# Kernel optimization log

Hardware: AMD Instinct MI355X
Metric: run time of the kernel (lower is better)

Reference implementation:

```python
import jax, jax.numpy as jnp
import numpy as np

N_PTS = 500000
R = 8            # channels per plane (num_channels=24 // 3)
FEAT = 24        # concat of 3 planes
HID = 168        # mlp_dim
OUT = 35
SIZES = [128, 256, 512]  # plane resolutions per level (plane_size=512, level_factor=0.5)
XYZ_MIN, XYZ_MAX = -2.0, 2.0


def setup_inputs() -> dict:
    key = jax.random.key(0)
    ks = jax.random.split(key, 64)
    inp = {"xyz": jax.random.uniform(ks[0], (N_PTS, 3), dtype=jnp.float32)}
    ki = 1
    for i, s in enumerate(SIZES):
        # planes stored [R, H, W]; torch init randn*0.1
        inp[f"xy{i}"] = jax.random.normal(ks[ki + 0], (R, s, s), dtype=jnp.float32) * 0.1
        inp[f"xz{i}"] = jax.random.normal(ks[ki + 1], (R, s, s), dtype=jnp.float32) * 0.1
        inp[f"yz{i}"] = jax.random.normal(ks[ki + 2], (R, s, s), dtype=jnp.float32) * 0.1
        inp[f"w1_{i}"] = jax.random.normal(ks[ki + 3], (FEAT, HID), dtype=jnp.float32) * 0.05
        inp[f"b1_{i}"] = jnp.zeros((HID,), jnp.float32)
        inp[f"w2_{i}"] = jax.random.normal(ks[ki + 4], (HID, HID), dtype=jnp.float32) * 0.05
        inp[f"b2_{i}"] = jnp.zeros((HID,), jnp.float32)
        inp[f"w3_{i}"] = jax.random.normal(ks[ki + 5], (HID, OUT), dtype=jnp.float32) * 0.05
        inp[f"b3_{i}"] = jnp.zeros((OUT,), jnp.float32)
        ki += 6
    return inp


def _bilinear(plane, gx, gy):
    # plane: [C,H,W]; gx in [-1,1] maps to W, gy maps to H; align_corners=True
    C, H, W = plane.shape
    ix = (gx + 1.0) * 0.5 * (W - 1)
    iy = (gy + 1.0) * 0.5 * (H - 1)
    x0 = jnp.floor(ix).astype(jnp.int32)
    y0 = jnp.floor(iy).astype(jnp.int32)
    wx = ix - x0
    wy = iy - y0
    x0c = jnp.clip(x0, 0, W - 1); x1c = jnp.clip(x0 + 1, 0, W - 1)
    y0c = jnp.clip(y0, 0, H - 1); y1c = jnp.clip(y0 + 1, 0, H - 1)
    v00 = plane[:, y0c, x0c]  # [C,N]
    v01 = plane[:, y0c, x1c]
    v10 = plane[:, y1c, x0c]
    v11 = plane[:, y1c, x1c]
    top = v00 * (1 - wx) + v01 * wx
    bot = v10 * (1 - wx) + v11 * wx
    return (top * (1 - wy) + bot * wy).T  # [N,C]


def _forward(xyz, planes, mlps):
    nrm = (xyz - XYZ_MIN) / (XYZ_MAX - XYZ_MIN) * 2.0 - 1.0  # [N,3]
    nx, ny, nz = nrm[:, 0], nrm[:, 1], nrm[:, 2]
    tmp = 0.0
    for (xy, xz, yz), (w1, b1, w2, b2, w3, b3) in zip(planes, mlps):
        # xy_plane[H=X,W=Y] sampled with grid (gx=ny, gy=nx), etc.
        feat = jnp.concatenate([
            _bilinear(xy, ny, nx),
            _bilinear(xz, nz, nx),
            _bilinear(yz, nz, ny),
        ], axis=-1)  # [N,24]
        h = jax.nn.relu(feat @ w1 + b1)
        h = jax.nn.relu(h @ w2 + b2)
        tmp = tmp + (h @ w3 + b3)
    # inference head: features[:27], rotations[27:31] raw; scale sigmoid; opacity*10
    return jnp.concatenate([tmp[:, :31], jax.nn.sigmoid(tmp[:, 31:34]), tmp[:, 34:] * 10.0], axis=-1)


def reference(xyz, xy0, xz0, yz0, w1_0, b1_0, w2_0, b2_0, w3_0, b3_0,
              xy1, xz1, yz1, w1_1, b1_1, w2_1, b2_1, w3_1, b3_1,
              xy2, xz2, yz2, w1_2, b1_2, w2_2, b2_2, w3_2, b3_2):
    planes = [(xy0, xz0, yz0), (xy1, xz1, yz1), (xy2, xz2, yz2)]
    mlps = [(w1_0, b1_0, w2_0, b2_0, w3_0, b3_0),
            (w1_1, b1_1, w2_1, b2_1, w3_1, b3_1),
            (w1_2, b1_2, w2_2, b2_2, w3_2, b3_2)]
    return _forward(xyz, planes, mlps)
```

## Files before the change

kernel.cpp:

```cpp
#include <hip/hip_runtime.h>

#define N_PTS 500000
#define FEAT 24
#define HID 168
#define OUT_C 35
#define MT 64
#define H_STR 176
#define WREG (32 * H_STR + 16)

#define WF1_OFF 0
#define WF2_OFF 18432
#define WF3_OFF 129024
#define W_TOTAL 156672
#define PL_S0 (W_TOTAL)
#define PL_S1 (PL_S0 + 393216)
#define PL_S2 (PL_S1 + 1572864)

typedef short bf16x8 __attribute__((ext_vector_type(8)));
typedef float f32x4 __attribute__((ext_vector_type(4)));

__device__ __forceinline__ unsigned short f2bf(float f) {
    union { float f; unsigned int u; } v; v.f = f;
    unsigned int u = v.u;
    return (unsigned short)((u + 0x7FFFu + ((u >> 16) & 1u)) >> 16);
}
__device__ __forceinline__ float bf2f(unsigned short h) {
    union { unsigned int u; float f; } v; v.u = ((unsigned int)h) << 16;
    return v.f;
}
__device__ __forceinline__ unsigned int pk_bf16(float a, float b) {
    unsigned int r;
    asm("v_cvt_pk_bf16_f32 %0, %1, %2" : "=v"(r) : "v"(a), "v"(b));
    return r;
}
__device__ __forceinline__ f32x4 mfma16(bf16x8 a, bf16x8 b, f32x4 c) {
    return __builtin_amdgcn_mfma_f32_16x16x32_bf16(a, b, c, 0, 0, 0);
}

__global__ __launch_bounds__(256) void prep_weights(
    const float* __restrict__ w1a, const float* __restrict__ w2a, const float* __restrict__ w3a,
    const float* __restrict__ w1b, const float* __restrict__ w2b, const float* __restrict__ w3b,
    const float* __restrict__ w1c, const float* __restrict__ w2c, const float* __restrict__ w3c,
    unsigned short* __restrict__ ws)
{
    int id = blockIdx.x * 256 + threadIdx.x;
    if (id >= W_TOTAL) return;
    const float* w1[3] = {w1a, w1b, w1c};
    const float* w2[3] = {w2a, w2b, w2c};
    const float* w3[3] = {w3a, w3b, w3c};
    float v = 0.f;
    if (id < WF2_OFF) {
        int s = id / 6144, r = id % 6144;
        int mt = r >> 9, q = r & 511, lane = q >> 3, j = q & 7;
        int n = mt * 16 + (lane & 15), k = (lane >> 4) * 8 + j;
        if (n < HID && k < FEAT) v = w1[s][k * HID + n];
    } else if (id < WF3_OFF) {
        int t = id - WF2_OFF;
        int s = t / 36864, r = t % 36864;
        int fi = r >> 9, q = r & 511, lane = q >> 3, j = q & 7;
        int kk = fi / 12, mt = fi % 12;
        int n = mt * 16 + (lane & 15), k = kk * 32 + (lane >> 4) * 8 + j;
        if (n < HID && k < HID) v = w2[s][k * HID + n];
    } else {
        int t = id - WF3_OFF;
        int s = t / 9216, r = t % 9216;
        int fi = r >> 9, q = r & 511, lane = q >> 3, j = q & 7;
        int mt = fi / 6, kk = fi % 6;
        int n = mt * 16 + (lane & 15), k = kk * 32 + (lane >> 4) * 8 + j;
        if (n < OUT_C && k < HID) v = w3[s][k * OUT_C + n];
    }
    ws[id] = f2bf(v);
}

__global__ __launch_bounds__(256) void prep_planes(
    const float* __restrict__ xy0, const float* __restrict__ xz0, const float* __restrict__ yz0,
    const float* __restrict__ xy1, const float* __restrict__ xz1, const float* __restrict__ yz1,
    const float* __restrict__ xy2, const float* __restrict__ xz2, const float* __restrict__ yz2,
    unsigned short* __restrict__ ws)
{
    const float* pls[9] = {xy0, xz0, yz0, xy1, xz1, yz1, xy2, xz2, yz2};
    int b = blockIdx.x;
    int s, pl, chunk, SS, base;
    if (b < 192)        { s = 0; SS = 16384;  pl = b / 64;   chunk = b % 64;    base = PL_S0; }
    else if (b < 960)   { int t = b - 192; s = 1; SS = 65536;  pl = t / 256;  chunk = t % 256;  base = PL_S1; }
    else                { int t = b - 960; s = 2; SS = 262144; pl = t / 1024; chunk = t % 1024; base = PL_S2; }
    const float* src = pls[s * 3 + pl];
    int pos = chunk * 256 + threadIdx.x;
    uint4 pk;
    unsigned int* po = (unsigned int*)&pk;
    #pragma unroll
    for (int c = 0; c < 4; ++c) {
        float f0 = src[(2 * c)     * SS + pos];
        float f1 = src[(2 * c + 1) * SS + pos];
        po[c] = pk_bf16(f0, f1);
    }
    *reinterpret_cast<uint4*>(&ws[base + pl * SS * 8 + pos * 8]) = pk;
}

__global__ __launch_bounds__(128, 4) void tri_mlp(
    const float* __restrict__ xyz,
    const float* __restrict__ b1_0, const float* __restrict__ b2_0, const float* __restrict__ b3_0,
    const float* __restrict__ b1_1, const float* __restrict__ b2_1, const float* __restrict__ b3_1,
    const float* __restrict__ b1_2, const float* __restrict__ b2_2, const float* __restrict__ b3_2,
    const unsigned short* __restrict__ wpack,
    float* __restrict__ out)
{
    __shared__ __align__(16) unsigned short H[2 * WREG];

    const int tid  = threadIdx.x;
    const int wave = tid >> 6;
    const int lane = tid & 63;
    const int quad = lane >> 4;
    const int l16  = lane & 15;
    const int p0   = blockIdx.x * MT;
    const int prow = wave * 32;
    unsigned short* Hw = H + wave * WREG;

    if (lane < 8) ((unsigned int*)(Hw + 32 * H_STR))[lane] = 0u;

    float X[2], Y[2], Z[2];
    #pragma unroll
    for (int ni = 0; ni < 2; ++ni) {
        int gp = min(p0 + prow + ni * 16 + l16, N_PTS - 1);
        X[ni] = xyz[gp * 3 + 0];
        Y[ni] = xyz[gp * 3 + 1];
        Z[ni] = xyz[gp * 3 + 2];
    }

    f32x4 c3[2][3];
    #pragma unroll
    for (int mt = 0; mt < 3; ++mt) {
        f32x4 cb;
        #pragma unroll
        for (int r = 0; r < 4; ++r) {
            int ch = mt * 16 + quad * 4 + r;
            cb[r] = (ch < OUT_C) ? (b3_0[ch] + b3_1[ch] + b3_2[ch]) : 0.f;
        }
        c3[0][mt] = cb;
        c3[1][mt] = cb;
    }

    #pragma unroll 1
    for (int s = 0; s < 3; ++s) {
        const float *b1, *b2;
        int S, sbase;
        if (s == 0)      { b1 = b1_0; b2 = b2_0; S = 128; sbase = PL_S0; }
        else if (s == 1) { b1 = b1_1; b2 = b2_1; S = 256; sbase = PL_S1; }
        else             { b1 = b1_2; b2 = b2_2; S = 512; sbase = PL_S2; }

        bf16x8 B1[2];
        #pragma unroll
        for (int ni = 0; ni < 2; ++ni) {
            uint4 pk = {0u, 0u, 0u, 0u};
            if (quad < 3) {
                float gx, gy;
                if (quad == 0)      { gx = Y[ni]; gy = X[ni]; }
                else if (quad == 1) { gx = Z[ni]; gy = X[ni]; }
                else                { gx = Z[ni]; gy = Y[ni]; }
                gx *= 0.5f; gy *= 0.5f;
                float ix = (gx + 1.0f) * 0.5f * (float)(S - 1);
                float iy = (gy + 1.0f) * 0.5f * (float)(S - 1);
                float fx = floorf(ix), fy = floorf(iy);
                int x0 = (int)fx, y0 = (int)fy;
                float wx = ix - fx, wy = iy - fy;
                int x0c = min(max(x0, 0), S - 1);
                int x1c = min(x0 + 1, S - 1);
                int y0c = min(max(y0, 0), S - 1);
                int y1c = min(y0 + 1, S - 1);
                const unsigned short* pcl = wpack + sbase + (quad << 3) * S * S;
                uint4 q00 = *(const uint4*)&pcl[(y0c * S + x0c) * 8];
                uint4 q01 = *(const uint4*)&pcl[(y0c * S + x1c) * 8];
                uint4 q10 = *(const uint4*)&pcl[(y1c * S + x0c) * 8];
                uint4 q11 = *(const uint4*)&pcl[(y1c * S + x1c) * 8];
                float w00 = (1.f - wx) * (1.f - wy), w01 = wx * (1.f - wy);
                float w10 = (1.f - wx) * wy,         w11 = wx * wy;
                const unsigned int* u00 = (const unsigned int*)&q00;
                const unsigned int* u01 = (const unsigned int*)&q01;
                const unsigned int* u10 = (const unsigned int*)&q10;
                const unsigned int* u11 = (const unsigned int*)&q11;
                unsigned int* po = (unsigned int*)&pk;
                #pragma unroll
                for (int h = 0; h < 4; ++h) {
                    float a0 = bf2f((unsigned short)(u00[h] & 0xFFFF)) * w00
                             + bf2f((unsigned short)(u01[h] & 0xFFFF)) * w01
                             + bf2f((unsigned short)(u10[h] & 0xFFFF)) * w10
                             + bf2f((unsigned short)(u11[h] & 0xFFFF)) * w11;
                    float a1 = bf2f((unsigned short)(u00[h] >> 16)) * w00
                             + bf2f((unsigned short)(u01[h] >> 16)) * w01
                             + bf2f((unsigned short)(u10[h] >> 16)) * w10
                             + bf2f((unsigned short)(u11[h] >> 16)) * w11;
                    po[h] = pk_bf16(a0, a1);
                }
            }
            B1[ni] = *reinterpret_cast<bf16x8*>(&pk);
        }

        {
            const unsigned short* w1f = wpack + WF1_OFF + s * 6144;
            #pragma unroll
            for (int mt = 0; mt < 11; ++mt) {
                bf16x8 a = *(const bf16x8*)&w1f[mt * 512 + lane * 8];
                float4 bias = *(const float4*)&b1[min(mt * 16 + quad * 4, HID - 4)];
                f32x4 cb = {bias.x, bias.y, bias.z, bias.w};
                #pragma unroll
                for (int ni = 0; ni < 2; ++ni) {
                    f32x4 c = mfma16(a, B1[ni], cb);
                    unsigned int u0 = pk_bf16(fmaxf(c[0], 0.f), fmaxf(c[1], 0.f));
                    unsigned int u1 = pk_bf16(fmaxf(c[2], 0.f), fmaxf(c[3], 0.f));
                    *reinterpret_cast<uint2*>(&Hw[(ni * 16 + l16) * H_STR + mt * 16 + quad * 4]) =
                        make_uint2(u0, u1);
                }
            }
        }

        bf16x8 B2[2][6];
        #pragma unroll
        for (int ni = 0; ni < 2; ++ni)
            #pragma unroll
            for (int kk = 0; kk < 6; ++kk)
                B2[ni][kk] = *(const bf16x8*)&Hw[(ni * 16 + l16) * H_STR + kk * 32 + quad * 8];

        {
            const unsigned short* w2f = wpack + WF2_OFF + s * 36864;
            #pragma unroll 1
            for (int mt = 0; mt < 11; ++mt) {
                float4 bias = *(const float4*)&b2[min(mt * 16 + quad * 4, HID - 4)];
                f32x4 c20 = {bias.x, bias.y, bias.z, bias.w};
                f32x4 c21 = c20;
                #pragma unroll
                for (int kk = 0; kk < 6; ++kk) {
                    bf16x8 a = *(const bf16x8*)&w2f[(kk * 12 + mt) * 512 + lane * 8];
                    c20 = mfma16(a, B2[0][kk], c20);
                    c21 = mfma16(a, B2[1][kk], c21);
                }
                unsigned int u00 = pk_bf16(fmaxf(c20[0], 0.f), fmaxf(c20[1], 0.f));
                unsigned int u01 = pk_bf16(fmaxf(c20[2], 0.f), fmaxf(c20[3], 0.f));
                *reinterpret_cast<uint2*>(&Hw[(l16) * H_STR + mt * 16 + quad * 4]) =
                    make_uint2(u00, u01);
                unsigned int u10 = pk_bf16(fmaxf(c21[0], 0.f), fmaxf(c21[1], 0.f));
                unsigned int u11 = pk_bf16(fmaxf(c21[2], 0.f), fmaxf(c21[3], 0.f));
                *reinterpret_cast<uint2*>(&Hw[(16 + l16) * H_STR + mt * 16 + quad * 4]) =
                    make_uint2(u10, u11);
            }
        }

        {
            const unsigned short* w3f = wpack + WF3_OFF + s * 9216;
            #pragma unroll 1
            for (int kk = 0; kk < 6; ++kk) {
                bf16x8 b30 = *(const bf16x8*)&Hw[(l16) * H_STR + kk * 32 + quad * 8];
                bf16x8 b31 = *(const bf16x8*)&Hw[(16 + l16) * H_STR + kk * 32 + quad * 8];
                #pragma unroll
                for (int mt = 0; mt < 3; ++mt) {
                    bf16x8 a = *(const bf16x8*)&w3f[(mt * 6 + kk) * 512 + lane * 8];
                    c3[0][mt] = mfma16(a, b30, c3[0][mt]);
                    c3[1][mt] = mfma16(a, b31, c3[1][mt]);
                }
            }
        }
    }

    float* Hf = (float*)Hw;
    #pragma unroll
    for (int ni = 0; ni < 2; ++ni) {
        int row = ni * 16 + l16;
        #pragma unroll
        for (int mt = 0; mt < 3; ++mt) {
            #pragma unroll
            for (int r = 0; r < 4; ++r) {
                int ch = mt * 16 + quad * 4 + r;
                if (ch < OUT_C) {
                    float v = c3[ni][mt][r];
                    if (ch >= 31 && ch < 34)      v = 1.0f / (1.0f + expf(-v));
                    else if (ch == 34)            v *= 10.0f;
                    Hf[row * 35 + ch] = v;
                }
            }
        }
    }
    if (p0 + prow < N_PTS) {
        const int base = (p0 + prow) * 35;
        #pragma unroll
        for (int t = 0; t < 5; ++t) {
            int off = t * 256 + lane * 4;
            if (off < 1120) {
                f32x4 v = *(const f32x4*)&Hf[off];
                __builtin_nontemporal_store(v, reinterpret_cast<f32x4*>(&out[base + off]));
            }
        }
    }
}

extern "C" void kernel_launch(void* const* d_in, const int* in_sizes, int n_in,
                              void* d_out, int out_size, void* d_ws, size_t ws_size,
                              hipStream_t stream) {
    (void)in_sizes; (void)n_in; (void)out_size; (void)ws_size;
    const float* xyz  = (const float*)d_in[0];
    const float* xy0  = (const float*)d_in[1];
    const float* xz0  = (const float*)d_in[2];
    const float* yz0  = (const float*)d_in[3];
    const float* w1_0 = (const float*)d_in[4];
    const float* b1_0 = (const float*)d_in[5];
    const float* w2_0 = (const float*)d_in[6];
    const float* b2_0 = (const float*)d_in[7];
    const float* w3_0 = (const float*)d_in[8];
    const float* b3_0 = (const float*)d_in[9];
    const float* xy1  = (const float*)d_in[10];
    const float* xz1  = (const float*)d_in[11];
    const float* yz1  = (const float*)d_in[12];
    const float* w1_1 = (const float*)d_in[13];
    const float* b1_1 = (const float*)d_in[14];
    const float* w2_1 = (const float*)d_in[15];
    const float* b2_1 = (const float*)d_in[16];
    const float* w3_1 = (const float*)d_in[17];
    const float* b3_1 = (const float*)d_in[18];
    const float* xy2  = (const float*)d_in[19];
    const float* xz2  = (const float*)d_in[20];
    const float* yz2  = (const float*)d_in[21];
    const float* w1_2 = (const float*)d_in[22];
    const float* b1_2 = (const float*)d_in[23];
    const float* w2_2 = (const float*)d_in[24];
    const float* b2_2 = (const float*)d_in[25];
    const float* w3_2 = (const float*)d_in[26];
    const float* b3_2 = (const float*)d_in[27];

    unsigned short* ws = (unsigned short*)d_ws;
    float* out = (float*)d_out;

    prep_weights<<<(W_TOTAL + 255) / 256, 256, 0, stream>>>(
        w1_0, w2_0, w3_0, w1_1, w2_1, w3_1, w1_2, w2_2, w3_2, ws);

    prep_planes<<<4032, 256, 0, stream>>>(
        xy0, xz0, yz0, xy1, xz1, yz1, xy2, xz2, yz2, ws);

    tri_mlp<<<(N_PTS + MT - 1) / MT, 128, 0, stream>>>(
        xyz,
        b1_0, b2_0, b3_0, b1_1, b2_1, b3_1, b1_2, b2_2, b3_2,
        ws, out);
}
```

Before: 374.2 us.

## Fold MLP biases into padded weight K-slot and merge prep kernels

```diff
diff --git a/kernel.cpp b/kernel.cpp
--- a/kernel.cpp
+++ b/kernel.cpp
@@ -16,6 +16,8 @@
 #define PL_S1 (PL_S0 + 393216)
 #define PL_S2 (PL_S1 + 1572864)
 
+#define PREP_W_BLOCKS 612
+
 typedef short bf16x8 __attribute__((ext_vector_type(8)));
 typedef float f32x4 __attribute__((ext_vector_type(4)));
 
@@ -37,49 +39,62 @@
     return __builtin_amdgcn_mfma_f32_16x16x32_bf16(a, b, c, 0, 0, 0);
 }
 
-__global__ __launch_bounds__(256) void prep_weights(
+__global__ __launch_bounds__(256) void prep_all(
+    const float* __restrict__ xy0, const float* __restrict__ xz0, const float* __restrict__ yz0,
+    const float* __restrict__ xy1, const float* __restrict__ xz1, const float* __restrict__ yz1,
+    const float* __restrict__ xy2, const float* __restrict__ xz2, const float* __restrict__ yz2,
     const float* __restrict__ w1a, const float* __restrict__ w2a, const float* __restrict__ w3a,
     const float* __restrict__ w1b, const float* __restrict__ w2b, const float* __restrict__ w3b,
     const float* __restrict__ w1c, const float* __restrict__ w2c, const float* __restrict__ w3c,
+    const float* __restrict__ b1a, const float* __restrict__ b2a, const float* __restrict__ b3a,
+    const float* __restrict__ b1b, const float* __restrict__ b2b, const float* __restrict__ b3b,
+    const float* __restrict__ b1c, const float* __restrict__ b2c, const float* __restrict__ b3c,
     unsigned short* __restrict__ ws)
 {
-    int id = blockIdx.x * 256 + threadIdx.x;
-    if (id >= W_TOTAL) return;
-    const float* w1[3] = {w1a, w1b, w1c};
-    const float* w2[3] = {w2a, w2b, w2c};
-    const float* w3[3] = {w3a, w3b, w3c};
-    float v = 0.f;
-    if (id < WF2_OFF) {
-        int s = id / 6144, r = id % 6144;
-        int mt = r >> 9, q = r & 511, lane = q >> 3, j = q & 7;
-        int n = mt * 16 + (lane & 15), k = (lane >> 4) * 8 + j;
-        if (n < HID && k < FEAT) v = w1[s][k * HID + n];
-    } else if (id < WF3_OFF) {
-        int t = id - WF2_OFF;
-        int s = t / 36864, r = t % 36864;
-        int fi = r >> 9, q = r & 511, lane = q >> 3, j = q & 7;
-        int kk = fi / 12, mt = fi % 12;
-        int n = mt * 16 + (lane & 15), k = kk * 32 + (lane >> 4) * 8 + j;
-        if (n < HID && k < HID) v = w2[s][k * HID + n];
-    } else {
-        int t = id - WF3_OFF;
-        int s = t / 9216, r = t % 9216;
-        int fi = r >> 9, q = r & 511, lane = q >> 3, j = q & 7;
-        int mt = fi / 6, kk = fi % 6;
-        int n = mt * 16 + (lane & 15), k = kk * 32 + (lane >> 4) * 8 + j;
-        if (n < OUT_C && k < HID) v = w3[s][k * OUT_C + n];
-    }
-    ws[id] = f2bf(v);
-}
-
-__global__ __launch_bounds__(256) void prep_planes(
-    const float* __restrict__ xy0, const float* __restrict__ xz0, const float* __restrict__ yz0,
-    const float* __restrict__ xy1, const float* __restrict__ xz1, const float* __restrict__ yz1,
-    const float* __restrict__ xy2, const float* __restrict__ xz2, const float* __restrict__ yz2,
-    unsigned short* __restrict__ ws)
-{
+    if (blockIdx.x < PREP_W_BLOCKS) {
+        int id = blockIdx.x * 256 + threadIdx.x;
+        const float* w1[3] = {w1a, w1b, w1c};
+        const float* w2[3] = {w2a, w2b, w2c};
+        const float* w3[3] = {w3a, w3b, w3c};
+        const float* b1[3] = {b1a, b1b, b1c};
+        const float* b2[3] = {b2a, b2b, b2c};
+        const float* b3[3] = {b3a, b3b, b3c};
+        float v = 0.f;
+        if (id < WF2_OFF) {
+            int s = id / 6144, r = id % 6144;
+            int mt = r >> 9, q = r & 511, lane = q >> 3, j = q & 7;
+            int n = mt * 16 + (lane & 15), k = (lane >> 4) * 8 + j;
+            if (n < HID) {
+                if (k < FEAT)       v = w1[s][k * HID + n];
+                else if (k == FEAT) v = b1[s][n];
+            }
+        } else if (id < WF3_OFF) {
+            int t = id - WF2_OFF;
+            int s = t / 36864, r = t % 36864;
+            int fi = r >> 9, q = r & 511, lane = q >> 3, j = q & 7;
+            int kk = fi / 12, mt = fi % 12;
+            int n = mt * 16 + (lane & 15), k = kk * 32 + (lane >> 4) * 8 + j;
+            if (n < HID) {
+                if (k < HID)        v = w2[s][k * HID + n];
+                else if (k == HID)  v = b2[s][n];
+            }
+        } else {
+            int t = id - WF3_OFF;
+            int s = t / 9216, r = t % 9216;
+            int fi = r >> 9, q = r & 511, lane = q >> 3, j = q & 7;
+            int mt = fi / 6, kk = fi % 6;
+            int n = mt * 16 + (lane & 15), k = kk * 32 + (lane >> 4) * 8 + j;
+            if (n < OUT_C) {
+                if (k < HID)        v = w3[s][k * OUT_C + n];
+                else if (k == HID)  v = b3[s][n];
+            }
+        }
+        ws[id] = f2bf(v);
+        return;
+    }
+
     const float* pls[9] = {xy0, xz0, yz0, xy1, xz1, yz1, xy2, xz2, yz2};
-    int b = blockIdx.x;
+    int b = blockIdx.x - PREP_W_BLOCKS;
     int s, pl, chunk, SS, base;
     if (b < 192)        { s = 0; SS = 16384;  pl = b / 64;   chunk = b % 64;    base = PL_S0; }
     else if (b < 960)   { int t = b - 192; s = 1; SS = 65536;  pl = t / 256;  chunk = t % 256;  base = PL_S1; }
@@ -99,9 +114,6 @@
 
 __global__ __launch_bounds__(128, 4) void tri_mlp(
     const float* __restrict__ xyz,
-    const float* __restrict__ b1_0, const float* __restrict__ b2_0, const float* __restrict__ b3_0,
-    const float* __restrict__ b1_1, const float* __restrict__ b2_1, const float* __restrict__ b3_1,
-    const float* __restrict__ b1_2, const float* __restrict__ b2_2, const float* __restrict__ b3_2,
     const unsigned short* __restrict__ wpack,
     float* __restrict__ out)
 {
@@ -116,6 +128,8 @@
     const int prow = wave * 32;
     unsigned short* Hw = H + wave * WREG;
 
+    if (lane < 32)
+        *reinterpret_cast<uint4*>(&Hw[lane * H_STR + HID]) = make_uint4(0x3F80u, 0u, 0u, 0u);
     if (lane < 8) ((unsigned int*)(Hw + 32 * H_STR))[lane] = 0u;
 
     float X[2], Y[2], Z[2];
@@ -130,28 +144,21 @@
     f32x4 c3[2][3];
     #pragma unroll
     for (int mt = 0; mt < 3; ++mt) {
-        f32x4 cb;
-        #pragma unroll
-        for (int r = 0; r < 4; ++r) {
-            int ch = mt * 16 + quad * 4 + r;
-            cb[r] = (ch < OUT_C) ? (b3_0[ch] + b3_1[ch] + b3_2[ch]) : 0.f;
-        }
-        c3[0][mt] = cb;
-        c3[1][mt] = cb;
+        c3[0][mt] = (f32x4){0.f, 0.f, 0.f, 0.f};
+        c3[1][mt] = (f32x4){0.f, 0.f, 0.f, 0.f};
     }
 
     #pragma unroll 1
     for (int s = 0; s < 3; ++s) {
-        const float *b1, *b2;
         int S, sbase;
-        if (s == 0)      { b1 = b1_0; b2 = b2_0; S = 128; sbase = PL_S0; }
-        else if (s == 1) { b1 = b1_1; b2 = b2_1; S = 256; sbase = PL_S1; }
-        else             { b1 = b1_2; b2 = b2_2; S = 512; sbase = PL_S2; }
+        if (s == 0)      { S = 128; sbase = PL_S0; }
+        else if (s == 1) { S = 256; sbase = PL_S1; }
+        else             { S = 512; sbase = PL_S2; }
 
         bf16x8 B1[2];
         #pragma unroll
         for (int ni = 0; ni < 2; ++ni) {
-            uint4 pk = {0u, 0u, 0u, 0u};
+            uint4 pk = {0x3F80u, 0u, 0u, 0u};
             if (quad < 3) {
                 float gx, gy;
                 if (quad == 0)      { gx = Y[ni]; gy = X[ni]; }
@@ -200,15 +207,14 @@
             #pragma unroll
             for (int mt = 0; mt < 11; ++mt) {
                 bf16x8 a = *(const bf16x8*)&w1f[mt * 512 + lane * 8];
-                float4 bias = *(const float4*)&b1[min(mt * 16 + quad * 4, HID - 4)];
-                f32x4 cb = {bias.x, bias.y, bias.z, bias.w};
                 #pragma unroll
                 for (int ni = 0; ni < 2; ++ni) {
-                    f32x4 c = mfma16(a, B1[ni], cb);
+                    f32x4 c = mfma16(a, B1[ni], (f32x4){0.f, 0.f, 0.f, 0.f});
                     unsigned int u0 = pk_bf16(fmaxf(c[0], 0.f), fmaxf(c[1], 0.f));
                     unsigned int u1 = pk_bf16(fmaxf(c[2], 0.f), fmaxf(c[3], 0.f));
-                    *reinterpret_cast<uint2*>(&Hw[(ni * 16 + l16) * H_STR + mt * 16 + quad * 4]) =
-                        make_uint2(u0, u1);
+                    if (mt < 10 || quad < 2)
+                        *reinterpret_cast<uint2*>(&Hw[(ni * 16 + l16) * H_STR + mt * 16 + quad * 4]) =
+                            make_uint2(u0, u1);
                 }
             }
         }
@@ -224,8 +230,7 @@
             const unsigned short* w2f = wpack + WF2_OFF + s * 36864;
             #pragma unroll 1
             for (int mt = 0; mt < 11; ++mt) {
-                float4 bias = *(const float4*)&b2[min(mt * 16 + quad * 4, HID - 4)];
-                f32x4 c20 = {bias.x, bias.y, bias.z, bias.w};
+                f32x4 c20 = {0.f, 0.f, 0.f, 0.f};
                 f32x4 c21 = c20;
                 #pragma unroll
                 for (int kk = 0; kk < 6; ++kk) {
@@ -233,14 +238,16 @@
                     c20 = mfma16(a, B2[0][kk], c20);
                     c21 = mfma16(a, B2[1][kk], c21);
                 }
-                unsigned int u00 = pk_bf16(fmaxf(c20[0], 0.f), fmaxf(c20[1], 0.f));
-                unsigned int u01 = pk_bf16(fmaxf(c20[2], 0.f), fmaxf(c20[3], 0.f));
-                *reinterpret_cast<uint2*>(&Hw[(l16) * H_STR + mt * 16 + quad * 4]) =
-                    make_uint2(u00, u01);
-                unsigned int u10 = pk_bf16(fmaxf(c21[0], 0.f), fmaxf(c21[1], 0.f));
-                unsigned int u11 = pk_bf16(fmaxf(c21[2], 0.f), fmaxf(c21[3], 0.f));
-                *reinterpret_cast<uint2*>(&Hw[(16 + l16) * H_STR + mt * 16 + quad * 4]) =
-                    make_uint2(u10, u11);
+                if (mt < 10 || quad < 2) {
+                    unsigned int u00 = pk_bf16(fmaxf(c20[0], 0.f), fmaxf(c20[1], 0.f));
+                    unsigned int u01 = pk_bf16(fmaxf(c20[2], 0.f), fmaxf(c20[3], 0.f));
+                    *reinterpret_cast<uint2*>(&Hw[(l16) * H_STR + mt * 16 + quad * 4]) =
+                        make_uint2(u00, u01);
+                    unsigned int u10 = pk_bf16(fmaxf(c21[0], 0.f), fmaxf(c21[1], 0.f));
+                    unsigned int u11 = pk_bf16(fmaxf(c21[2], 0.f), fmaxf(c21[3], 0.f));
+                    *reinterpret_cast<uint2*>(&Hw[(16 + l16) * H_STR + mt * 16 + quad * 4]) =
+                        make_uint2(u10, u11);
+                }
             }
         }
 
@@ -327,14 +334,11 @@
     unsigned short* ws = (unsigned short*)d_ws;
     float* out = (float*)d_out;
 
-    prep_weights<<<(W_TOTAL + 255) / 256, 256, 0, stream>>>(
-        w1_0, w2_0, w3_0, w1_1, w2_1, w3_1, w1_2, w2_2, w3_2, ws);
-
-    prep_planes<<<4032, 256, 0, stream>>>(
-        xy0, xz0, yz0, xy1, xz1, yz1, xy2, xz2, yz2, ws);
-
-    tri_mlp<<<(N_PTS + MT - 1) / MT, 128, 0, stream>>>(
-        xyz,
+    prep_all<<<PREP_W_BLOCKS + 4032, 256, 0, stream>>>(
+        xy0, xz0, yz0, xy1, xz1, yz1, xy2, xz2, yz2,
+        w1_0, w2_0, w3_0, w1_1, w2_1, w3_1, w1_2, w2_2, w3_2,
         b1_0, b2_0, b3_0, b1_1, b2_1, b3_1, b1_2, b2_2, b3_2,
-        ws, out);
-}
+        ws);
+
+    tri_mlp<<<(N_PTS + MT - 1) / MT, 128, 0, stream>>>(xyz, ws, out);
+}
```

After: 351.6 us. 1.06x faster.
